# Kernel optimization log

Measured on AMD Instinct MI355X. Metric: run time of the kernel, lower is better.

## Reference

```python
import jax, jax.numpy as jnp
import numpy as np

B, S, H, D = 4, 2048, 16, 1024  # batch, seq, heads, n_units
DK = D // H


def setup_inputs() -> dict:
    key = jax.random.key(0)
    ks = jax.random.split(key, 12)
    k_init = float(np.sqrt(1.0 / D))
    u = lambda k, shape: jax.random.uniform(k, shape, jnp.float32, -k_init, k_init)
    # causal mask, shared across batch/heads (True = attend)
    mask = jnp.broadcast_to(jnp.tril(jnp.ones((S, S), dtype=bool)), (B, S, S))
    return {
        "query": jax.random.normal(ks[0], (B, S, D), jnp.float32),
        "key": jax.random.normal(ks[1], (B, S, D), jnp.float32),
        "value": jax.random.normal(ks[2], (B, S, D), jnp.float32),
        "Wq": u(ks[3], (H, DK, D)), "bq": u(ks[4], (H, DK)),
        "Wk": u(ks[5], (H, DK, D)), "bk": u(ks[6], (H, DK)),
        "Wv": u(ks[7], (H, DK, D)), "bv": u(ks[8], (H, DK)),
        "Wp": u(ks[9], (D, D)), "bp": u(ks[10], (D,)),
        "mask": mask,
    }


def reference(query, key, value, Wq, bq, Wk, bk, Wv, bv, Wp, bp, mask):
    # per-head projections, batched over heads: [B,S,D] x [H,DK,D] -> [B,H,S,DK]
    Q = jnp.einsum('bsd,hkd->bhsk', query, Wq) + bq[None, :, None, :]
    K = jnp.einsum('bsd,hkd->bhsk', key, Wk) + bk[None, :, None, :]
    V = jnp.einsum('bsd,hkd->bhsk', value, Wv) + bv[None, :, None, :]
    scores = jnp.einsum('bhsk,bhtk->bhst', Q, K) / jnp.sqrt(jnp.float32(DK))
    scores = jnp.where(mask[:, None, :, :], scores, jnp.float32(-1e9))
    attn = jax.nn.softmax(scores, axis=-1)  # dropout disabled (eval)
    Z = jnp.einsum('bhst,bhtk->bhsk', attn, V)
    # concat heads on feature dim: [B,S,H*DK]
    Z = jnp.transpose(Z, (0, 2, 1, 3)).reshape(B, S, D)
    return Z @ Wp.T + bp
```

## Files before the change

kernel.cpp:

```cpp
#include <hip/hip_runtime.h>

typedef __bf16 bf16;
typedef __bf16 bf16x8 __attribute__((ext_vector_type(8)));
typedef float f32x4 __attribute__((ext_vector_type(4)));

#define BB 4
#define SS 2048
#define HH 16
#define DD 1024
#define DK 64
#define MTOT (BB * SS)

#define C1 0.18033688f
#define C2 -11.5415603f

__device__ __forceinline__ void gl_lds16(const bf16* g, bf16* l)
{
    __builtin_amdgcn_global_load_lds(
        (const __attribute__((address_space(1))) unsigned int*)g,
        (__attribute__((address_space(3))) unsigned int*)l, 16, 0, 0);
}

__global__ __launch_bounds__(256) void conv_kernel(
    const float* __restrict__ q, const float* __restrict__ k,
    const float* __restrict__ v,
    const float* __restrict__ wq, const float* __restrict__ wk,
    const float* __restrict__ wv, const float* __restrict__ wp,
    bf16* __restrict__ xdst, bf16* __restrict__ wdst)
{
    const float* src; bf16* d; size_t i;
    if (blockIdx.z < 3) {
        src = (blockIdx.z == 0) ? q : (blockIdx.z == 1) ? k : v;
        d = xdst + (size_t)blockIdx.z * ((size_t)MTOT * DD);
        i = ((size_t)blockIdx.x * 256 + threadIdx.x) * 8;
    } else {
        if (blockIdx.x >= 2048) return;
        const int wsel = blockIdx.x >> 9;
        src = (wsel == 0) ? wq : (wsel == 1) ? wk : (wsel == 2) ? wv : wp;
        d = wdst + (size_t)wsel * ((size_t)DD * DD);
        i = ((size_t)(blockIdx.x & 511) * 256 + threadIdx.x) * 8;
    }
    const float4 v0 = *(const float4*)(src + i);
    const float4 v1 = *(const float4*)(src + i + 4);
    bf16x8 r = { (bf16)v0.x, (bf16)v0.y, (bf16)v0.z, (bf16)v0.w,
                 (bf16)v1.x, (bf16)v1.y, (bf16)v1.z, (bf16)v1.w };
    *(bf16x8*)(d + i) = r;
}

template<int KC, int NH>
__device__ __forceinline__ void qphase(
    const bf16* __restrict__ sb, int wm, int wn, int lr, int swz8,
    bf16x8 a[8], f32x4 acc[8][4],
    const bf16* __restrict__ ssrc, bf16* __restrict__ sdst, bool doStage)
{
    if constexpr (NH == 0) {
        #pragma unroll
        for (int i = 0; i < 8; ++i)
            a[i] = *(const bf16x8*)&sb[KC * 8192 + (wm * 128 + i * 16 + lr) * 32 + swz8];
    }
    bf16x8 b0 = *(const bf16x8*)&sb[16384 + KC * 8192 + (wn * 64 + (NH * 2 + 0) * 16 + lr) * 32 + swz8];
    bf16x8 b1 = *(const bf16x8*)&sb[16384 + KC * 8192 + (wn * 64 + (NH * 2 + 1) * 16 + lr) * 32 + swz8];
    __builtin_amdgcn_s_barrier();
    asm volatile("s_waitcnt lgkmcnt(0)" ::: "memory");
    __builtin_amdgcn_s_setprio(1);
    #pragma unroll
    for (int i = 0; i < 8; ++i) {
        acc[i][NH * 2 + 0] = __builtin_amdgcn_mfma_f32_16x16x32_bf16(
                                 a[i], b0, acc[i][NH * 2 + 0], 0, 0, 0);
        acc[i][NH * 2 + 1] = __builtin_amdgcn_mfma_f32_16x16x32_bf16(
                                 a[i], b1, acc[i][NH * 2 + 1], 0, 0, 0);
    }
    __builtin_amdgcn_s_setprio(0);
    if (doStage) {
        gl_lds16(ssrc, sdst);
        gl_lds16(ssrc + (size_t)128 * DD, sdst + 4096);
    }
}

__global__ __launch_bounds__(512, 2) void gemm_qkv(
    const bf16* __restrict__ x0, const bf16* __restrict__ x1,
    const bf16* __restrict__ x2, const bf16* __restrict__ w0,
    const bf16* __restrict__ w1, const bf16* __restrict__ w2,
    const float* __restrict__ bias0, const float* __restrict__ bias1,
    const float* __restrict__ bias2,
    bf16* __restrict__ o0, bf16* __restrict__ o1, bf16* __restrict__ o2)
{
    __shared__ __align__(16) bf16 smem[2 * 32768];

    const int z = blockIdx.z;
    const bf16* A = (z == 0) ? x0 : (z == 1) ? x1 : x2;
    const bf16* W = (z == 0) ? w0 : (z == 1) ? w1 : w2;
    const float* bias = (z == 0) ? bias0 : (z == 1) ? bias1 : bias2;
    bf16* out = (z == 0) ? o0 : (z == 1) ? o1 : o2;

    const int tid  = threadIdx.x;
    const int w    = tid >> 6;
    const int lane = tid & 63;
    const int quad = lane >> 4;
    const int lr   = lane & 15;
    const int wm   = w >> 2;
    const int wn   = w & 3;

    const int m_base = blockIdx.y * 256;
    const int n_base = blockIdx.x * 256;
    const int swz8 = (quad ^ ((lr >> 1) & 3)) * 8;

    const int c0 = ((tid & 3) ^ ((tid >> 3) & 3)) * 8;
    const bf16* srcA = A + (size_t)(m_base + (tid >> 2)) * DD + c0;
    const bf16* srcB = W + (size_t)(n_base + (tid >> 2)) * DD + c0;

    f32x4 acc[8][4];
    #pragma unroll
    for (int i = 0; i < 8; ++i)
        #pragma unroll
        for (int j = 0; j < 4; ++j)
            acc[i][j] = (f32x4){0.f, 0.f, 0.f, 0.f};
    bf16x8 a[8];

    #pragma unroll
    for (int t = 0; t < 2; ++t) {
        bf16* db = smem + t * 32768;
        #pragma unroll
        for (int kc = 0; kc < 2; ++kc) {
            const bf16* sA = srcA + t * 64 + kc * 32;
            const bf16* sB = srcB + t * 64 + kc * 32;
            gl_lds16(sA,                      db + kc * 8192 + w * 512);
            gl_lds16(sA + (size_t)128 * DD,   db + kc * 8192 + 4096 + w * 512);
            gl_lds16(sB,                      db + 16384 + kc * 8192 + w * 512);
            gl_lds16(sB + (size_t)128 * DD,   db + 16384 + kc * 8192 + 4096 + w * 512);
        }
    }
    asm volatile("s_waitcnt vmcnt(8)" ::: "memory");
    __builtin_amdgcn_s_barrier();

    #pragma unroll 2
    for (int T = 0; T < 16; ++T) {
        const bf16* sb = smem + (T & 1) * 32768;
        bf16* db = smem + (T & 1) * 32768;
        const bool st = (T + 2 < 16);
        const int tn = st ? (T + 2) : 0;
        const bf16* sA = srcA + tn * 64;
        const bf16* sB = srcB + tn * 64;

        qphase<0, 0>(sb, wm, wn, lr, swz8, a, acc, sA,      db + w * 512,                 st);
        __builtin_amdgcn_s_barrier();
        qphase<0, 1>(sb, wm, wn, lr, swz8, a, acc, sB,      db + 16384 + w * 512,         st);
        __builtin_amdgcn_s_barrier();
        qphase<1, 0>(sb, wm, wn, lr, swz8, a, acc, sA + 32, db + 8192 + w * 512,          st);
        __builtin_amdgcn_s_barrier();
        qphase<1, 1>(sb, wm, wn, lr, swz8, a, acc, sB + 32, db + 16384 + 8192 + w * 512,  st);
        if (st) asm volatile("s_waitcnt vmcnt(8)" ::: "memory");
        else    asm volatile("s_waitcnt vmcnt(0)" ::: "memory");
        __builtin_amdgcn_s_barrier();
    }

    if (z == 2) {
        bf16* e = smem + w * 2176;
        const int hh = (n_base + wn * 64) >> 6;
        const int mg = m_base + wm * 128;
        const int b  = mg >> 11;
        const int s0 = mg & (SS - 1);
        #pragma unroll
        for (int j = 0; j < 4; ++j) {
            const float bb = bias[n_base + wn * 64 + j * 16 + lr];
            #pragma unroll
            for (int i = 0; i < 8; ++i)
                #pragma unroll
                for (int r = 0; r < 4; ++r)
                    e[lr * 136 + i * 16 + quad * 4 + r] = (bf16)(acc[i][j][r] + bb);
            #pragma unroll
            for (int p = 0; p < 4; ++p) {
                const int nn = p * 4 + quad;
                const int mm = lr * 8;
                const bf16x8 vv = *(const bf16x8*)&e[nn * 136 + mm];
                const int dk = j * 16 + nn;
                *(bf16x8*)(out + ((size_t)(b * HH + hh) * DK + dk) * SS + s0 + mm) = vv;
            }
        }
    } else {
        #pragma unroll
        for (int j = 0; j < 4; ++j) {
            const int n  = n_base + wn * 64 + j * 16 + lr;
            const float bb = bias[n];
            const int hh = n >> 6;
            const int dk = n & (DK - 1);
            #pragma unroll
            for (int i = 0; i < 8; ++i)
                #pragma unroll
                for (int r = 0; r < 4; ++r) {
                    const int m = m_base + wm * 128 + i * 16 + quad * 4 + r;
                    const int bi = m >> 11, s = m & (SS - 1);
                    out[(((size_t)bi * HH + hh) * SS + s) * DK + dk]
                        = (bf16)(acc[i][j][r] + bb);
                }
        }
    }
}

__global__ __launch_bounds__(256) void gemm_out(
    const bf16* __restrict__ A, const bf16* __restrict__ W,
    const float* __restrict__ bias, float* __restrict__ out)
{
    __shared__ __align__(16) bf16 As[128 * 32];
    __shared__ __align__(16) bf16 Bs[64 * 32];

    const int tid  = threadIdx.x;
    const int wave = tid >> 6;
    const int lane = tid & 63;
    const int quad = lane >> 4;
    const int lr   = lane & 15;

    const int m_base = blockIdx.y * 128;
    const int n_base = blockIdx.x * 64;
    const int srow = lane >> 2;
    const int scol = (lane & 3) * 8;

    f32x4 acc[2][4];
    #pragma unroll
    for (int i = 0; i < 2; ++i)
        #pragma unroll
        for (int j = 0; j < 4; ++j)
            acc[i][j] = (f32x4){0.f, 0.f, 0.f, 0.f};

    for (int k0 = 0; k0 < DD; k0 += 32) {
        #pragma unroll
        for (int seg = wave; seg < 12; seg += 4) {
            if (seg < 8)
                gl_lds16(A + (size_t)(m_base + seg * 16 + srow) * DD + k0 + scol,
                         As + seg * 512);
            else
                gl_lds16(W + (size_t)(n_base + (seg - 8) * 16 + srow) * DD + k0 + scol,
                         Bs + (seg - 8) * 512);
        }
        __syncthreads();

        bf16x8 af[2], bfr[4];
        #pragma unroll
        for (int i = 0; i < 2; ++i)
            af[i] = *(const bf16x8*)&As[(wave * 32 + i * 16 + lr) * 32 + quad * 8];
        #pragma unroll
        for (int j = 0; j < 4; ++j)
            bfr[j] = *(const bf16x8*)&Bs[(j * 16 + lr) * 32 + quad * 8];

        #pragma unroll
        for (int i = 0; i < 2; ++i)
            #pragma unroll
            for (int j = 0; j < 4; ++j)
                acc[i][j] = __builtin_amdgcn_mfma_f32_16x16x32_bf16(
                                af[i], bfr[j], acc[i][j], 0, 0, 0);
        __syncthreads();
    }

    #pragma unroll
    for (int j = 0; j < 4; ++j) {
        const int n = n_base + j * 16 + lr;
        const float bb = bias[n];
        #pragma unroll
        for (int i = 0; i < 2; ++i)
            #pragma unroll
            for (int r = 0; r < 4; ++r) {
                const int m = m_base + wave * 32 + i * 16 + quad * 4 + r;
                out[(size_t)m * DD + n] = acc[i][j][r] + bb;
            }
    }
}

template <bool DIAG>
__device__ __forceinline__ void attn_tile4(
    int quad, int lr, const bf16* __restrict__ Kc, const bf16* __restrict__ Vc,
    bf16* __restrict__ pb, const bf16x8 aq[2][2], const bf16x8& ones,
    f32x4 acc[2][4], f32x4 acc_l[2])
{
    bf16x8 kb[2][2];
    #pragma unroll
    for (int kvh = 0; kvh < 2; ++kvh)
        #pragma unroll
        for (int kc = 0; kc < 2; ++kc)
            kb[kvh][kc] = *(const bf16x8*)&Kc[
                ((kvh * 16 + lr) * 8 + ((kc * 4 + quad) ^ (lr & 7))) * 8];
    bf16x8 vb[4];
    #pragma unroll
    for (int c = 0; c < 4; ++c)
        vb[c] = *(const bf16x8*)&Vc[
            ((c * 16 + lr) * 4 + (quad ^ ((lr >> 1) & 3))) * 8];

    f32x4 s[2][2];
    #pragma unroll
    for (int h = 0; h < 2; ++h)
        #pragma unroll
        for (int kvh = 0; kvh < 2; ++kvh) {
            s[h][kvh] = (f32x4){0.f, 0.f, 0.f, 0.f};
            s[h][kvh] = __builtin_amdgcn_mfma_f32_16x16x32_bf16(
                            aq[h][0], kb[kvh][0], s[h][kvh], 0, 0, 0);
            s[h][kvh] = __builtin_amdgcn_mfma_f32_16x16x32_bf16(
                            aq[h][1], kb[kvh][1], s[h][kvh], 0, 0, 0);
        }

    #pragma unroll
    for (int h = 0; h < 2; ++h)
        #pragma unroll
        for (int kvh = 0; kvh < 2; ++kvh)
            #pragma unroll
            for (int r = 0; r < 4; ++r) {
                float p = exp2f(fmaf(s[h][kvh][r], C1, C2));
                if constexpr (DIAG) {
                    const bool ok = (kvh * 16 + lr) <= (h * 16 + quad * 4 + r);
                    p = ok ? p : 0.0f;
                }
                pb[(h * 16 + quad * 4 + r) * 40 + kvh * 16 + lr] = (bf16)p;
            }

    bf16x8 ap[2];
    #pragma unroll
    for (int h = 0; h < 2; ++h)
        ap[h] = *(const bf16x8*)&pb[(h * 16 + lr) * 40 + quad * 8];

    #pragma unroll
    for (int h = 0; h < 2; ++h)
        acc_l[h] = __builtin_amdgcn_mfma_f32_16x16x32_bf16(
                        ap[h], ones, acc_l[h], 0, 0, 0);
    #pragma unroll
    for (int c = 0; c < 4; ++c)
        #pragma unroll
        for (int h = 0; h < 2; ++h)
            acc[h][c] = __builtin_amdgcn_mfma_f32_16x16x32_bf16(
                            ap[h], vb[c], acc[h][c], 0, 0, 0);
}

__global__ __launch_bounds__(256, 4) void attn_kernel4(
    const bf16* __restrict__ q_ws, const bf16* __restrict__ k_ws,
    const bf16* __restrict__ v_ws, bf16* __restrict__ z_ws)
{
    __shared__ __align__(16) bf16 Kst[2][32 * 64];
    __shared__ __align__(16) bf16 Vst[2][64 * 32];
    __shared__ __align__(16) bf16 pbuf[4][32 * 40];

    const int tid  = threadIdx.x;
    const int w    = tid >> 6;
    const int lane = tid & 63;
    const int quad = lane >> 4;
    const int lr   = lane & 15;

    const int bh = blockIdx.x & 63;
    const int qg = 15 - (blockIdx.x >> 6);
    const int m0 = qg * 128 + w * 32;
    const int lim = 4 * qg + w;
    const int ntiles = 4 * qg + 4;

    const size_t base = (size_t)bh * SS * DK;
    const bf16* Kb = k_ws + base;
    const bf16* Vb = v_ws + base;
    bf16* pb = pbuf[w];

    const int krow = w * 8 + (lane >> 3);
    const int kcc  = (lane & 7) ^ ((lane >> 3) & 7);
    const bf16* ksrc = Kb + (size_t)krow * DK + kcc * 8;
    const int vrow = w * 16 + (lane >> 2);
    const int vcc  = (lane & 3) ^ ((lane >> 3) & 3);
    const bf16* vsrc = Vb + (size_t)vrow * SS + vcc * 8;

    bf16x8 aq[2][2];
    #pragma unroll
    for (int h = 0; h < 2; ++h)
        #pragma unroll
        for (int kc = 0; kc < 2; ++kc)
            aq[h][kc] = *(const bf16x8*)(q_ws + base
                + (size_t)(m0 + h * 16 + lr) * DK + kc * 32 + quad * 8);

    bf16x8 ones;
    #pragma unroll
    for (int i = 0; i < 8; ++i) ones[i] = (bf16)1.0f;

    f32x4 acc[2][4], acc_l[2];
    #pragma unroll
    for (int h = 0; h < 2; ++h) {
        acc_l[h] = (f32x4){0.f, 0.f, 0.f, 0.f};
        #pragma unroll
        for (int c = 0; c < 4; ++c) acc[h][c] = (f32x4){0.f, 0.f, 0.f, 0.f};
    }

    gl_lds16(ksrc, &Kst[0][w * 512]);
    gl_lds16(vsrc, &Vst[0][w * 512]);
    __syncthreads();

    for (int t = 0; t < ntiles; ++t) {
        if (t + 1 < ntiles) {
            gl_lds16(ksrc + (size_t)(t + 1) * 32 * DK, &Kst[(t + 1) & 1][w * 512]);
            gl_lds16(vsrc + (t + 1) * 32,              &Vst[(t + 1) & 1][w * 512]);
        }
        const bf16* Kc = Kst[t & 1];
        const bf16* Vc = Vst[t & 1];
        if (t < lim)
            attn_tile4<false>(quad, lr, Kc, Vc, pb, aq, ones, acc, acc_l);
        else if (t == lim)
            attn_tile4<true>(quad, lr, Kc, Vc, pb, aq, ones, acc, acc_l);
        __syncthreads();
    }

    const int b = bh >> 4, hh = bh & (HH - 1);
    #pragma unroll
    for (int h = 0; h < 2; ++h)
        #pragma unroll
        for (int r = 0; r < 4; ++r) {
            const float inv = 1.0f / acc_l[h][r];
            const int s = m0 + h * 16 + quad * 4 + r;
            #pragma unroll
            for (int c = 0; c < 4; ++c)
                z_ws[((size_t)(b * SS + s)) * DD + hh * DK + c * 16 + lr]
                    = (bf16)(acc[h][c][r] * inv);
        }
}

extern "C" void kernel_launch(void* const* d_in, const int* in_sizes, int n_in,
                              void* d_out, int out_size, void* d_ws, size_t ws_size,
                              hipStream_t stream)
{
    const float* query = (const float*)d_in[0];
    const float* key_  = (const float*)d_in[1];
    const float* value = (const float*)d_in[2];
    const float* Wq = (const float*)d_in[3];
    const float* bq = (const float*)d_in[4];
    const float* Wk = (const float*)d_in[5];
    const float* bk = (const float*)d_in[6];
    const float* Wv = (const float*)d_in[7];
    const float* bv = (const float*)d_in[8];
    const float* Wp = (const float*)d_in[9];
    const float* bp = (const float*)d_in[10];

    const size_t X = (size_t)MTOT * DD;
    const size_t W = (size_t)DD * DD;
    bf16* xq  = (bf16*)d_ws;
    bf16* xk  = xq + X;
    bf16* xv  = xk + X;
    bf16* wqb = xv + X;
    bf16* wkb = wqb + W;
    bf16* wvb = wkb + W;
    bf16* wpb = wvb + W;
    bf16* q_ws = wpb + W;
    bf16* k_ws = q_ws + X;
    bf16* v_ws = k_ws + X;
    bf16* z_ws = xq;

    conv_kernel<<<dim3(4096, 1, 4), 256, 0, stream>>>(
        query, key_, value, Wq, Wk, Wv, Wp, xq, wqb);

    gemm_qkv<<<dim3(4, 32, 3), 512, 0, stream>>>(
        xq, xk, xv, wqb, wkb, wvb, bq, bk, bv, q_ws, k_ws, v_ws);

    attn_kernel4<<<dim3(1024), 256, 0, stream>>>(q_ws, k_ws, v_ws, z_ws);

    gemm_out<<<dim3(16, 64), 256, 0, stream>>>(z_ws, wpb, bp, (float*)d_out);
}
```

Baseline: 368.3 us.

## Rewrite output projection GEMM with larger tiles and double-buffered async LDS pipeline

The output projection GEMM moves from a 128x64 tile with four waves and a synchronous load-then-compute loop to a 256x128 tile with eight waves. It now double-buffers swizzled LDS stages loaded by global_load_lds, using the same phased structure as the QKV GEMM. Scheduling barriers are also added around the waitcnt and barrier in the QKV GEMM phases to keep the compiler from reordering. The aim is to hide global load latency and improve operand reuse, at the cost of more LDS and register use per block and fewer blocks (256) across the CUs.

```diff
diff --git a/kernel.cpp b/kernel.cpp
--- a/kernel.cpp
+++ b/kernel.cpp
@@ -60,8 +60,10 @@
     }
     bf16x8 b0 = *(const bf16x8*)&sb[16384 + KC * 8192 + (wn * 64 + (NH * 2 + 0) * 16 + lr) * 32 + swz8];
     bf16x8 b1 = *(const bf16x8*)&sb[16384 + KC * 8192 + (wn * 64 + (NH * 2 + 1) * 16 + lr) * 32 + swz8];
+    __builtin_amdgcn_sched_barrier(0);
     __builtin_amdgcn_s_barrier();
     asm volatile("s_waitcnt lgkmcnt(0)" ::: "memory");
+    __builtin_amdgcn_sched_barrier(0);
     __builtin_amdgcn_s_setprio(1);
     #pragma unroll
     for (int i = 0; i < 8; ++i) {
@@ -75,6 +77,7 @@
         gl_lds16(ssrc, sdst);
         gl_lds16(ssrc + (size_t)128 * DD, sdst + 4096);
     }
+    __builtin_amdgcn_sched_barrier(0);
 }
 
 __global__ __launch_bounds__(512, 2) void gemm_qkv(
@@ -197,69 +200,110 @@
     }
 }
 
-__global__ __launch_bounds__(256) void gemm_out(
+template<int KC>
+__device__ __forceinline__ void ophase(
+    const bf16* __restrict__ sb, int wm, int wn, int lr, int swz8,
+    f32x4 acc[4][4],
+    const bf16* __restrict__ sA, const bf16* __restrict__ sB,
+    bf16* __restrict__ db, int w, bool doStage)
+{
+    bf16x8 a[4], b[4];
+    #pragma unroll
+    for (int i = 0; i < 4; ++i)
+        a[i] = *(const bf16x8*)&sb[KC * 8192 + (wm * 64 + i * 16 + lr) * 32 + swz8];
+    #pragma unroll
+    for (int j = 0; j < 4; ++j)
+        b[j] = *(const bf16x8*)&sb[16384 + KC * 4096 + (wn * 64 + j * 16 + lr) * 32 + swz8];
+    __builtin_amdgcn_sched_barrier(0);
+    __builtin_amdgcn_s_barrier();
+    asm volatile("s_waitcnt lgkmcnt(0)" ::: "memory");
+    __builtin_amdgcn_sched_barrier(0);
+    __builtin_amdgcn_s_setprio(1);
+    #pragma unroll
+    for (int i = 0; i < 4; ++i)
+        #pragma unroll
+        for (int j = 0; j < 4; ++j)
+            acc[i][j] = __builtin_amdgcn_mfma_f32_16x16x32_bf16(
+                            a[i], b[j], acc[i][j], 0, 0, 0);
+    __builtin_amdgcn_s_setprio(0);
+    if (doStage) {
+        gl_lds16(sA + KC * 32,                    db + KC * 8192 + w * 512);
+        gl_lds16(sA + KC * 32 + (size_t)128 * DD, db + KC * 8192 + 4096 + w * 512);
+        gl_lds16(sB + KC * 32,                    db + 16384 + KC * 4096 + w * 512);
+    }
+    __builtin_amdgcn_sched_barrier(0);
+}
+
+__global__ __launch_bounds__(512, 2) void gemm_out(
     const bf16* __restrict__ A, const bf16* __restrict__ W,
     const float* __restrict__ bias, float* __restrict__ out)
 {
-    __shared__ __align__(16) bf16 As[128 * 32];
-    __shared__ __align__(16) bf16 Bs[64 * 32];
+    __shared__ __align__(16) bf16 smem[2 * 24576];
 
     const int tid  = threadIdx.x;
-    const int wave = tid >> 6;
+    const int w    = tid >> 6;
     const int lane = tid & 63;
     const int quad = lane >> 4;
     const int lr   = lane & 15;
-
-    const int m_base = blockIdx.y * 128;
-    const int n_base = blockIdx.x * 64;
-    const int srow = lane >> 2;
-    const int scol = (lane & 3) * 8;
-
-    f32x4 acc[2][4];
-    #pragma unroll
-    for (int i = 0; i < 2; ++i)
+    const int wm   = w >> 1;
+    const int wn   = w & 1;
+
+    const int m_base = blockIdx.y * 256;
+    const int n_base = blockIdx.x * 128;
+    const int swz8 = (quad ^ ((lr >> 1) & 3)) * 8;
+
+    const int c0 = ((tid & 3) ^ ((tid >> 3) & 3)) * 8;
+    const bf16* srcA = A + (size_t)(m_base + (tid >> 2)) * DD + c0;
+    const bf16* srcB = W + (size_t)(n_base + (tid >> 2)) * DD + c0;
+
+    f32x4 acc[4][4];
+    #pragma unroll
+    for (int i = 0; i < 4; ++i)
         #pragma unroll
         for (int j = 0; j < 4; ++j)
             acc[i][j] = (f32x4){0.f, 0.f, 0.f, 0.f};
 
-    for (int k0 = 0; k0 < DD; k0 += 32) {
-        #pragma unroll
-        for (int seg = wave; seg < 12; seg += 4) {
-            if (seg < 8)
-                gl_lds16(A + (size_t)(m_base + seg * 16 + srow) * DD + k0 + scol,
-                         As + seg * 512);
-            else
-                gl_lds16(W + (size_t)(n_base + (seg - 8) * 16 + srow) * DD + k0 + scol,
-                         Bs + (seg - 8) * 512);
-        }
-        __syncthreads();
-
-        bf16x8 af[2], bfr[4];
-        #pragma unroll
-        for (int i = 0; i < 2; ++i)
-            af[i] = *(const bf16x8*)&As[(wave * 32 + i * 16 + lr) * 32 + quad * 8];
-        #pragma unroll
-        for (int j = 0; j < 4; ++j)
-            bfr[j] = *(const bf16x8*)&Bs[(j * 16 + lr) * 32 + quad * 8];
-
-        #pragma unroll
-        for (int i = 0; i < 2; ++i)
-            #pragma unroll
-            for (int j = 0; j < 4; ++j)
-                acc[i][j] = __builtin_amdgcn_mfma_f32_16x16x32_bf16(
-                                af[i], bfr[j], acc[i][j], 0, 0, 0);
-        __syncthreads();
+    #pragma unroll
+    for (int t = 0; t < 2; ++t) {
+        bf16* db = smem + t * 24576;
+        #pragma unroll
+        for (int kc = 0; kc < 2; ++kc) {
+            const bf16* sA = srcA + t * 64 + kc * 32;
+            const bf16* sB = srcB + t * 64 + kc * 32;
+            gl_lds16(sA,                      db + kc * 8192 + w * 512);
+            gl_lds16(sA + (size_t)128 * DD,   db + kc * 8192 + 4096 + w * 512);
+            gl_lds16(sB,                      db + 16384 + kc * 4096 + w * 512);
+        }
+    }
+    asm volatile("s_waitcnt vmcnt(6)" ::: "memory");
+    __builtin_amdgcn_s_barrier();
+
+    #pragma unroll 2
+    for (int T = 0; T < 16; ++T) {
+        const bf16* sb = smem + (T & 1) * 24576;
+        bf16* db = smem + (T & 1) * 24576;
+        const bool st = (T + 2 < 16);
+        const int tn = st ? (T + 2) : 0;
+        const bf16* sA = srcA + tn * 64;
+        const bf16* sB = srcB + tn * 64;
+
+        ophase<0>(sb, wm, wn, lr, swz8, acc, sA, sB, db, w, st);
+        __builtin_amdgcn_s_barrier();
+        ophase<1>(sb, wm, wn, lr, swz8, acc, sA, sB, db, w, st);
+        if (st) asm volatile("s_waitcnt vmcnt(6)" ::: "memory");
+        else    asm volatile("s_waitcnt vmcnt(0)" ::: "memory");
+        __builtin_amdgcn_s_barrier();
     }
 
     #pragma unroll
     for (int j = 0; j < 4; ++j) {
-        const int n = n_base + j * 16 + lr;
+        const int n = n_base + wn * 64 + j * 16 + lr;
         const float bb = bias[n];
         #pragma unroll
-        for (int i = 0; i < 2; ++i)
+        for (int i = 0; i < 4; ++i)
             #pragma unroll
             for (int r = 0; r < 4; ++r) {
-                const int m = m_base + wave * 32 + i * 16 + quad * 4 + r;
+                const int m = m_base + wm * 64 + i * 16 + quad * 4 + r;
                 out[(size_t)m * DD + n] = acc[i][j][r] + bb;
             }
     }
@@ -449,5 +493,5 @@
 
     attn_kernel4<<<dim3(1024), 256, 0, stream>>>(q_ws, k_ws, v_ws, z_ws);
 
-    gemm_out<<<dim3(16, 64), 256, 0, stream>>>(z_ws, wpb, bp, (float*)d_out);
-}
+    gemm_out<<<dim3(8, 32), 512, 0, stream>>>(z_ws, wpb, bp, (float*)d_out);
+}
```

Measured after the change: 355.8 us. -3.4%, faster.
